# Kernel optimization log

Measured on AMD Instinct MI355X. Metric: run time of the kernel, lower is better.

Reference implementation:

```python
import jax, jax.numpy as jnp
import numpy as np

HEADS = 6
DIM_HEAD = 64
SCALE = DIM_HEAD ** -0.5
BN_EPS = 1e-5


def _dw_pw(x, w_dw, gamma, beta, mean, var, w_pw, stride):
    """Depthwise 3x3 conv (groups=C) -> BatchNorm (inference) -> 1x1 pointwise conv."""
    C = x.shape[1]
    y = jax.lax.conv_general_dilated(
        x, w_dw, window_strides=(stride, stride), padding=((1, 1), (1, 1)),
        dimension_numbers=('NCHW', 'OIHW', 'NCHW'), feature_group_count=C)
    inv = gamma / jnp.sqrt(var + BN_EPS)
    y = y * inv[None, :, None, None] + (beta - mean * inv)[None, :, None, None]
    # 1x1 conv as einsum: w_pw is [O, C]
    return jnp.einsum('bchw,oc->bohw', y, w_pw)


def setup_inputs() -> dict:
    key = jax.random.key(0)
    ks = jax.random.split(key, 10)
    B, C, H, W = 32, 384, 32, 32
    inner = HEADS * DIM_HEAD  # 384
    ws = 0.05  # weight scale to keep attention logits sane
    return {
        'x': jax.random.normal(ks[0], (B, C, H, W), jnp.float32),
        'q_dw': jax.random.normal(ks[1], (C, 1, 3, 3), jnp.float32) * ws,
        'q_gamma': jnp.ones((C,), jnp.float32),
        'q_beta': jnp.zeros((C,), jnp.float32),
        'q_mean': jax.random.normal(ks[2], (C,), jnp.float32) * 0.1,
        'q_var': jax.random.uniform(ks[3], (C,), jnp.float32) + 0.5,
        'q_pw': jax.random.normal(ks[4], (inner, C), jnp.float32) * ws,
        'kv_dw': jax.random.normal(ks[5], (C, 1, 3, 3), jnp.float32) * ws,
        'kv_gamma': jnp.ones((C,), jnp.float32),
        'kv_beta': jnp.zeros((C,), jnp.float32),
        'kv_mean': jax.random.normal(ks[6], (C,), jnp.float32) * 0.1,
        'kv_var': jax.random.uniform(ks[7], (C,), jnp.float32) + 0.5,
        'kv_pw': jax.random.normal(ks[8], (2 * inner, C), jnp.float32) * ws,
        'out_w': jax.random.normal(ks[9], (C, inner), jnp.float32) * ws,
        'out_b': jnp.zeros((C,), jnp.float32),
    }


def reference(x, q_dw, q_gamma, q_beta, q_mean, q_var, q_pw,
              kv_dw, kv_gamma, kv_beta, kv_mean, kv_var, kv_pw,
              out_w, out_b):
    B, C, H, W = x.shape
    h, d = HEADS, DIM_HEAD
    # Q at full resolution, K/V spatially downsampled (stride 2)
    q = _dw_pw(x, q_dw, q_gamma, q_beta, q_mean, q_var, q_pw, stride=1)   # [B, h*d, H, W]
    kv = _dw_pw(x, kv_dw, kv_gamma, kv_beta, kv_mean, kv_var, kv_pw, stride=2)  # [B, 2*h*d, Hk, Wk]
    k, v = jnp.split(kv, 2, axis=1)
    Hk, Wk = k.shape[2], k.shape[3]
    # 'b (h d) x y -> b h (x y) d'
    q = q.reshape(B, h, d, H * W).transpose(0, 1, 3, 2)
    k = k.reshape(B, h, d, Hk * Wk).transpose(0, 1, 3, 2)
    v = v.reshape(B, h, d, Hk * Wk).transpose(0, 1, 3, 2)
    dots = jnp.einsum('bhid,bhjd->bhij', q, k) * SCALE  # [B, h, HW, HkWk]
    attn = jax.nn.softmax(dots, axis=-1)
    out = jnp.einsum('bhij,bhjd->bhid', attn, v)        # [B, h, HW, d]
    # 'b h (x y) d -> b (h d) x y'
    out = out.transpose(0, 1, 3, 2).reshape(B, h * d, H, W)
    # final 1x1 conv projection (dropout is identity, p=0)
    return jnp.einsum('bchw,oc->bohw', out, out_w) + out_b[None, :, None, None]
```

## Files before the change

### kernel.cpp

```cpp
#include <hip/hip_runtime.h>
#include <hip/hip_bf16.h>

#define CIN 384
#define PQ 1024
#define PKV 256
#define HEADS 6
#define DH 64
#define INNER 384
#define ATTN_SCALE 0.125f

typedef __hip_bfloat16 bf16;
typedef unsigned short ushort;
typedef __bf16 bf16x8 __attribute__((ext_vector_type(8)));
typedef float floatx4 __attribute__((ext_vector_type(4)));

__device__ __forceinline__ float b2f(bf16 v) { return __bfloat162float(v); }
__device__ __forceinline__ bf16 f2b(float v) { return __float2bfloat16(v); }
__device__ __forceinline__ ushort f2bu(float v) { bf16 h = __float2bfloat16(v); return *(ushort*)&h; }
__device__ __forceinline__ float ldf(const void* p, size_t i, int isbf) {
    return isbf ? __bfloat162float(((const bf16*)p)[i]) : ((const float*)p)[i];
}
__device__ __forceinline__ void dma16(const bf16* g, bf16* l) {
    __builtin_amdgcn_global_load_lds(
        (const __attribute__((address_space(1))) unsigned int*)g,
        (__attribute__((address_space(3))) unsigned int*)l, 16, 0, 0);
}
__device__ __forceinline__ int probe_isbf(const void* x) {
    const unsigned* u = (const unsigned*)x;
    int cnt = 0;
    for (int i = 0; i < 64; i++) {
        unsigned e = (u[i] >> 7) & 0xFFu;
        cnt += (e >= 100u && e <= 140u) ? 1 : 0;
    }
    return cnt >= 48 ? 1 : 0;
}
__device__ __forceinline__ unsigned cvtpk(float lo, float hi) {
    unsigned r;
    asm("v_cvt_pk_bf16_f32 %0, %1, %2" : "=v"(r) : "v"(lo), "v"(hi));
    return r;
}
__device__ __forceinline__ void halfswap(unsigned a, unsigned b, unsigned& lo, unsigned& hi) {
#if __has_builtin(__builtin_amdgcn_permlane32_swap)
    auto r = __builtin_amdgcn_permlane32_swap(a, b, false, false);
    lo = r[0]; hi = r[1];
#else
    unsigned ax = (unsigned)__shfl_xor((int)a, 32, 64);
    unsigned bx = (unsigned)__shfl_xor((int)b, 32, 64);
    bool lower = (threadIdx.x & 32) == 0;
    lo = lower ? a : bx;
    hi = lower ? ax : b;
#endif
}

__global__ void wconv_kernel(const void* __restrict__ w0, const void* __restrict__ w1,
                             const void* __restrict__ w2, bf16* __restrict__ dst,
                             const void* __restrict__ xprobe) {
    int isbf = probe_isbf(xprobe);
    const int n0 = INNER * CIN, n1 = 2 * INNER * CIN, n2 = INNER * CIN;
    int i = blockIdx.x * 256 + threadIdx.x;
    int total = n0 + n1 + n2;
    for (; i < total; i += gridDim.x * 256) {
        float v;
        if (i < n0) v = ldf(w0, i, isbf);
        else if (i < n0 + n1) v = ldf(w1, i - n0, isbf);
        else v = ldf(w2, i - n0 - n1, isbf);
        dst[i] = f2b(v);
    }
}

template <int STRIDE, int HO, int WO>
__global__ __launch_bounds__(256) void dw_bn_kernel(
        const void* __restrict__ x, const void* __restrict__ wdw,
        const void* __restrict__ gamma, const void* __restrict__ beta,
        const void* __restrict__ mean, const void* __restrict__ var,
        bf16* __restrict__ yt) {
    constexpr int IN_ROWS = (8 - 1) * STRIDE + 3;
    constexpr int RL = 37;
    constexpr int PT = 8 * WO;
    constexpr unsigned XSZ = 32u * IN_ROWS * RL * 4;
    constexpr unsigned OSZ = (unsigned)PT * 40 * 2;
    __shared__ __align__(16) char smem[XSZ > OSZ ? XSZ : OSZ];
    float (*xin)[IN_ROWS][RL] = (float (*)[IN_ROWS][RL])smem;
    ushort (*outt)[40] = (ushort (*)[40])smem;

    int isbf = probe_isbf(x);
    int rg = blockIdx.x;
    int c0 = blockIdx.y * 32;
    int b  = blockIdx.z;
    int tid = threadIdx.x;
    int ri0 = rg * 8 * STRIDE - 1;

    for (int e = tid; e < 32 * IN_ROWS; e += 256) {
        int i = e % IN_ROWS, cc = e / IN_ROWS;
        xin[cc][i][0] = 0.f;
        xin[cc][i][33] = 0.f;
    }

    const int NCHUNK = 32 * IN_ROWS * 4;
    for (int ch = tid; ch < NCHUNK; ch += 256) {
        int wc = ch & 3;
        int t  = ch >> 2;
        int i  = t % IN_ROWS;
        int cc = t / IN_ROWS;
        int row = ri0 + i;
        float f[8];
        if (row >= 0 && row < 32) {
            size_t goff = ((size_t)(b * CIN + c0 + cc) * 32 + row) * 32 + wc * 8;
            if (isbf) {
                uint4 v = *(const uint4*)((const bf16*)x + goff);
                const ushort* u = (const ushort*)&v;
#pragma unroll
                for (int j = 0; j < 8; j++) f[j] = __uint_as_float((unsigned)u[j] << 16);
            } else {
                float4 v0 = *(const float4*)((const float*)x + goff);
                float4 v1 = *(const float4*)((const float*)x + goff + 4);
                f[0] = v0.x; f[1] = v0.y; f[2] = v0.z; f[3] = v0.w;
                f[4] = v1.x; f[5] = v1.y; f[6] = v1.z; f[7] = v1.w;
            }
        } else {
#pragma unroll
            for (int j = 0; j < 8; j++) f[j] = 0.f;
        }
        float* dst = &xin[cc][i][1 + wc * 8];
#pragma unroll
        for (int j = 0; j < 8; j++) dst[j] = f[j];
    }

    int cc = tid & 31;
    int g  = tid >> 5;
    int c  = c0 + cc;
    float w9[9];
#pragma unroll
    for (int k = 0; k < 9; k++) w9[k] = ldf(wdw, c * 9 + k, isbf);
    float inv  = ldf(gamma, c, isbf) * rsqrtf(ldf(var, c, isbf) + 1e-5f);
    float bias = ldf(beta, c, isbf) - ldf(mean, c, isbf) * inv;
    __syncthreads();

    const float* xr0 = xin[cc][g * STRIDE + 0];
    const float* xr1 = xin[cc][g * STRIDE + 1];
    const float* xr2 = xin[cc][g * STRIDE + 2];
    float o[WO];
    if (STRIDE == 1) {
        float a0 = xr0[0], a1 = xr0[1];
        float b0 = xr1[0], b1 = xr1[1];
        float q0 = xr2[0], q1 = xr2[1];
#pragma unroll
        for (int wo = 0; wo < WO; wo++) {
            float a2 = xr0[wo + 2], b2 = xr1[wo + 2], q2 = xr2[wo + 2];
            float acc = w9[0] * a0 + w9[1] * a1 + w9[2] * a2
                      + w9[3] * b0 + w9[4] * b1 + w9[5] * b2
                      + w9[6] * q0 + w9[7] * q1 + w9[8] * q2;
            o[wo] = acc * inv + bias;
            a0 = a1; a1 = a2; b0 = b1; b1 = b2; q0 = q1; q1 = q2;
        }
    } else {
        float a0 = xr0[0], b0 = xr1[0], q0 = xr2[0];
#pragma unroll
        for (int wo = 0; wo < WO; wo++) {
            float a1 = xr0[2 * wo + 1], a2 = xr0[2 * wo + 2];
            float b1 = xr1[2 * wo + 1], b2 = xr1[2 * wo + 2];
            float q1 = xr2[2 * wo + 1], q2 = xr2[2 * wo + 2];
            float acc = w9[0] * a0 + w9[1] * a1 + w9[2] * a2
                      + w9[3] * b0 + w9[4] * b1 + w9[5] * b2
                      + w9[6] * q0 + w9[7] * q1 + w9[8] * q2;
            o[wo] = acc * inv + bias;
            a0 = a2; b0 = b2; q0 = q2;
        }
    }
    __syncthreads();

#pragma unroll
    for (int wo = 0; wo < WO; wo++) outt[g * WO + wo][cc] = f2bu(o[wo]);
    __syncthreads();

    const size_t pbase = (size_t)b * (HO * WO) + (size_t)rg * 8 * WO;
    for (int chk = tid; chk < PT * 4; chk += 256) {
        int k = chk & 3, p = chk >> 2;
        uint4 v = *(const uint4*)&outt[p][k * 8];
        *(uint4*)(yt + (pbase + p) * CIN + c0 + k * 8) = v;
    }
}

__global__ __launch_bounds__(256, 3) void mfma_pw_qkv(
        const bf16* __restrict__ qpw, const bf16* __restrict__ yqt,
        bf16* __restrict__ qalt,
        const bf16* __restrict__ kvpw, const bf16* __restrict__ ykvt,
        bf16* __restrict__ kalt, bf16* __restrict__ valt) {
    __shared__ __align__(16) bf16 As[2][4096];
    __shared__ __align__(16) bf16 Bs[2][4096];
    int tid = threadIdx.x;
    int wave = tid >> 6, lane = tid & 63;
    int l15 = lane & 15, quad = lane >> 4;
    int wm = wave & 1, wn = wave >> 1;

    int bid = blockIdx.x;
    int P, b, p0, o0;
    const bf16 *asrc0, *bsrc0;
    bf16* outq;
    if (bid < 768) {
        int m = bid;
        int p0t = m & 7; m >>= 3;
        int o0t = m % 3; b = m / 3;
        P = 1024; p0 = p0t * 128; o0 = o0t * 128;
        asrc0 = yqt; bsrc0 = qpw; outq = qalt;
    } else {
        int m = bid - 768;
        int p0t = m & 1; m >>= 1;
        int o0t = m % 6; b = m / 6;
        P = 256; p0 = p0t * 128; o0 = o0t * 128;
        asrc0 = ykvt; bsrc0 = kvpw; outq = kalt;
    }

    const bf16* asrc = asrc0 + ((size_t)b * P + p0) * CIN;
    const bf16* bsrc = bsrc0 + (size_t)o0 * CIN;

    int srow = (lane >> 2);
    int sc   = lane & 3;
    auto stage = [&](int step, int buf) {
#pragma unroll
        for (int it = 0; it < 2; it++) {
            int row = wave * 32 + it * 16 + srow;
            int g = sc ^ (row & 3);
            size_t goff = (size_t)row * CIN + step * 32 + g * 8;
            dma16(asrc + goff, &As[buf][(wave * 2 + it) * 512]);
            dma16(bsrc + goff, &Bs[buf][(wave * 2 + it) * 512]);
        }
    };

    floatx4 acc[4][4];
#pragma unroll
    for (int pt = 0; pt < 4; pt++)
#pragma unroll
        for (int ot = 0; ot < 4; ot++) acc[pt][ot] = (floatx4){0.f, 0.f, 0.f, 0.f};

    stage(0, 0);
    __syncthreads();
    for (int s = 0; s < CIN / 32; s++) {
        int buf = s & 1;
        if (s < CIN / 32 - 1) stage(s + 1, buf ^ 1);
        bf16x8 af[4], bw[4];
        int slot = (quad ^ (l15 & 3)) * 8;
#pragma unroll
        for (int pt = 0; pt < 4; pt++)
            af[pt] = *(const bf16x8*)&As[buf][(wm * 64 + pt * 16 + l15) * 32 + slot];
#pragma unroll
        for (int ot = 0; ot < 4; ot++)
            bw[ot] = *(const bf16x8*)&Bs[buf][(wn * 64 + ot * 16 + l15) * 32 + slot];
#pragma unroll
        for (int pt = 0; pt < 4; pt++)
#pragma unroll
            for (int ot = 0; ot < 4; ot++)
                acc[pt][ot] = __builtin_amdgcn_mfma_f32_16x16x32_bf16(af[pt], bw[ot], acc[pt][ot], 0, 0, 0);
        __syncthreads();
    }

    int pw0 = p0 + wm * 64, ow0 = o0 + wn * 64;
#pragma unroll
    for (int ot = 0; ot < 4; ot++) {
        int o = ow0 + ot * 16 + l15;
        if (o < INNER) {
            int h = o >> 6, d = o & 63;
            bf16* base = outq + ((size_t)(b * HEADS + h) * P) * 64 + d;
#pragma unroll
            for (int pt = 0; pt < 4; pt++)
#pragma unroll
                for (int r = 0; r < 4; r++)
                    base[(size_t)(pw0 + pt * 16 + quad * 4 + r) * 64] = f2b(acc[pt][ot][r]);
        } else {
            int ch = o - INNER;
            bf16* base = valt + ((size_t)b * INNER + ch) * PKV;
#pragma unroll
            for (int pt = 0; pt < 4; pt++)
#pragma unroll
                for (int r = 0; r < 4; r++)
                    base[pw0 + pt * 16 + quad * 4 + r] = f2b(acc[pt][ot][r]);
        }
    }
}

__global__ __launch_bounds__(256, 3) void mfma_pw_out(
        const bf16* __restrict__ wt, const bf16* __restrict__ yt,
        const void* __restrict__ bias, void* __restrict__ out0,
        const void* __restrict__ xprobe) {
    __shared__ __align__(16) bf16 As[2][4096];
    __shared__ __align__(16) bf16 Bs[2][4096];
    const int P = PQ, O = CIN;
    int tid = threadIdx.x;
    int wave = tid >> 6, lane = tid & 63;
    int l15 = lane & 15, quad = lane >> 4;
    int wm = wave & 1, wn = wave >> 1;
    int b = blockIdx.z;
    int p0 = blockIdx.x * 128;
    int o0 = blockIdx.y * 128;

    const bf16* asrc = yt + ((size_t)b * P + p0) * CIN;
    const bf16* bsrc = wt + (size_t)o0 * CIN;

    int srow = (lane >> 2);
    int sc   = lane & 3;
    auto stage = [&](int step, int buf) {
#pragma unroll
        for (int it = 0; it < 2; it++) {
            int row = wave * 32 + it * 16 + srow;
            int g = sc ^ (row & 3);
            size_t goff = (size_t)row * CIN + step * 32 + g * 8;
            dma16(asrc + goff, &As[buf][(wave * 2 + it) * 512]);
            dma16(bsrc + goff, &Bs[buf][(wave * 2 + it) * 512]);
        }
    };

    floatx4 acc[4][4];
#pragma unroll
    for (int pt = 0; pt < 4; pt++)
#pragma unroll
        for (int ot = 0; ot < 4; ot++) acc[pt][ot] = (floatx4){0.f, 0.f, 0.f, 0.f};

    stage(0, 0);
    __syncthreads();
    for (int s = 0; s < CIN / 32; s++) {
        int buf = s & 1;
        if (s < CIN / 32 - 1) stage(s + 1, buf ^ 1);
        bf16x8 af[4], bw[4];
        int slot = (quad ^ (l15 & 3)) * 8;
#pragma unroll
        for (int pt = 0; pt < 4; pt++)
            af[pt] = *(const bf16x8*)&As[buf][(wm * 64 + pt * 16 + l15) * 32 + slot];
#pragma unroll
        for (int ot = 0; ot < 4; ot++)
            bw[ot] = *(const bf16x8*)&Bs[buf][(wn * 64 + ot * 16 + l15) * 32 + slot];
#pragma unroll
        for (int pt = 0; pt < 4; pt++)
#pragma unroll
            for (int ot = 0; ot < 4; ot++)
                acc[pt][ot] = __builtin_amdgcn_mfma_f32_16x16x32_bf16(af[pt], bw[ot], acc[pt][ot], 0, 0, 0);
        __syncthreads();
    }

    int pw0 = p0 + wm * 64, ow0 = o0 + wn * 64;
    int isbf = probe_isbf(xprobe);
#pragma unroll
    for (int ot = 0; ot < 4; ot++) {
        int o = ow0 + ot * 16 + l15;
        float bv = ldf(bias, o, isbf);
#pragma unroll
        for (int pt = 0; pt < 4; pt++) {
            int p = pw0 + pt * 16 + quad * 4;
            size_t idx = ((size_t)b * O + o) * P + p;
            if (!isbf) {
                float4 v4 = {acc[pt][ot][0] + bv, acc[pt][ot][1] + bv,
                             acc[pt][ot][2] + bv, acc[pt][ot][3] + bv};
                *(float4*)((float*)out0 + idx) = v4;
            } else {
                ushort4 u4 = {f2bu(acc[pt][ot][0] + bv), f2bu(acc[pt][ot][1] + bv),
                              f2bu(acc[pt][ot][2] + bv), f2bu(acc[pt][ot][3] + bv)};
                *(ushort4*)((bf16*)out0 + idx) = u4;
            }
        }
    }
}

__global__ __launch_bounds__(256, 2) void attn_kernel(
        const bf16* __restrict__ qalt, const bf16* __restrict__ kalt,
        const bf16* __restrict__ valt, bf16* __restrict__ ao) {
    __shared__ __align__(16) bf16 Kl[16384];
    __shared__ __align__(16) bf16 Vl[16384];
    __shared__ __align__(16) ushort Ot[4][16][80];
    int tid = threadIdx.x;
    int wave = tid >> 6, lane = tid & 63;
    int l15 = lane & 15, quad = lane >> 4;
    int blk = blockIdx.x;
    int swz = (blk & 7) * 96 + (blk >> 3);
    int seg = swz & 3;
    int bh  = swz >> 2;
    int b = bh / HEADS, h = bh % HEADS;

    const bf16* qbase = qalt + (size_t)(b * HEADS + h) * PQ * DH;
    const bf16* kbase = kalt + (size_t)(b * HEADS + h) * PKV * DH;
    const bf16* vbase = valt + ((size_t)b * INNER + h * DH) * PKV;

    {
        int j = lane >> 3, cs = lane & 7;
#pragma unroll
        for (int it = 0; it < 8; it++) {
            int jr = (wave * 8 + it) * 8 + j;
            int g = cs ^ (jr & 7);
            dma16(kbase + (size_t)jr * 64 + g * 8, &Kl[(wave * 8 + it) * 512]);
        }
        int d = lane >> 5, cs2 = lane & 31;
#pragma unroll
        for (int it = 0; it < 8; it++) {
            int dr = (wave * 8 + it) * 2 + d;
            int g = cs2 ^ (dr & 15);
            dma16(vbase + (size_t)dr * 256 + g * 8, &Vl[(wave * 8 + it) * 512]);
        }
    }

    int p0 = seg * 256 + wave * 16;
    const bf16* qrow = qbase + (size_t)(p0 + l15) * DH + quad * 8;
    bf16x8 qc0 = *(const bf16x8*)qrow;
    bf16x8 qc1 = *(const bf16x8*)(qrow + 32);
    __syncthreads();

    const float C = ATTN_SCALE * 1.44269504f;

#pragma unroll
    for (int t = 0; t < 4; t++) {
        bf16x8 qn0 = qc0, qn1 = qc1;
        if (t < 3) {
            const bf16* qr = qrow + (size_t)(t + 1) * 64 * DH;
            qn0 = *(const bf16x8*)qr;
            qn1 = *(const bf16x8*)(qr + 32);
        }

        floatx4 s[16];
#pragma unroll
        for (int jt = 0; jt < 16; jt++) s[jt] = (floatx4){0.f, 0.f, 0.f, 0.f};
        __builtin_amdgcn_s_setprio(1);
#pragma unroll
        for (int jt = 0; jt < 16; jt++) {
            int j = jt * 16 + l15;
            bf16x8 k0 = *(const bf16x8*)&Kl[j * 64 + (quad ^ (j & 7)) * 8];
            bf16x8 k1 = *(const bf16x8*)&Kl[j * 64 + ((4 + quad) ^ (j & 7)) * 8];
            s[jt] = __builtin_amdgcn_mfma_f32_16x16x32_bf16(k0, qc0, s[jt], 0, 0, 0);
            s[jt] = __builtin_amdgcn_mfma_f32_16x16x32_bf16(k1, qc1, s[jt], 0, 0, 0);
        }
        __builtin_amdgcn_s_setprio(0);

        float mx = s[0][0];
#pragma unroll
        for (int jt = 0; jt < 16; jt++)
#pragma unroll
            for (int r = 0; r < 4; r++) mx = fmaxf(mx, s[jt][r]);
        mx = fmaxf(mx, __shfl_xor(mx, 16, 64));
        mx = fmaxf(mx, __shfl_xor(mx, 32, 64));
        float mc = mx * C;
        float sm = 0.f;
#pragma unroll
        for (int jt = 0; jt < 16; jt++)
#pragma unroll
            for (int r = 0; r < 4; r++) {
                float e = exp2f(s[jt][r] * C - mc);
                s[jt][r] = e;
                sm += e;
            }
        sm += __shfl_xor(sm, 16, 64);
        sm += __shfl_xor(sm, 32, 64);
        float pinv = 1.f / sm;

        floatx4 oacc[4];
#pragma unroll
        for (int nt = 0; nt < 4; nt++) oacc[nt] = (floatx4){0.f, 0.f, 0.f, 0.f};
        __builtin_amdgcn_s_setprio(1);
#pragma unroll
        for (int kk = 0; kk < 8; kk++) {
            floatx4 se = s[2 * kk], so = s[2 * kk + 1];
            unsigned E0 = cvtpk(se[0] * pinv, se[1] * pinv);
            unsigned E1 = cvtpk(se[2] * pinv, se[3] * pinv);
            unsigned D0 = cvtpk(so[0] * pinv, so[1] * pinv);
            unsigned D1 = cvtpk(so[2] * pinv, so[3] * pinv);
            unsigned lo0, hi0, lo1, hi1;
            halfswap(E0, D0, lo0, hi0);
            halfswap(E1, D1, lo1, hi1);
            unsigned sel0 = (quad & 1) ? hi0 : lo0;
            unsigned sel1 = (quad & 1) ? hi1 : lo1;
            unsigned x0 = (unsigned)__shfl_xor((int)sel0, 16, 64);
            unsigned x1 = (unsigned)__shfl_xor((int)sel1, 16, 64);
            union { unsigned u[4]; bf16x8 v; } pf;
            pf.u[0] = (quad & 1) ? x0 : sel0;
            pf.u[1] = (quad & 1) ? x1 : sel1;
            pf.u[2] = (quad & 1) ? sel0 : x0;
            pf.u[3] = (quad & 1) ? sel1 : x1;
#pragma unroll
            for (int nt = 0; nt < 4; nt++) {
                int d = nt * 16 + l15;
                bf16x8 bv = *(const bf16x8*)&Vl[d * 256 + ((kk * 4 + quad) ^ (d & 15)) * 8];
                oacc[nt] = __builtin_amdgcn_mfma_f32_16x16x32_bf16(pf.v, bv, oacc[nt], 0, 0, 0);
            }
        }
        __builtin_amdgcn_s_setprio(0);

#pragma unroll
        for (int nt = 0; nt < 4; nt++)
#pragma unroll
            for (int r = 0; r < 4; r++)
                Ot[wave][quad * 4 + r][nt * 16 + l15] = f2bu(oacc[nt][r]);
        int row = lane >> 2, d0 = (lane & 3) * 16;
        uint4 ld0 = *(const uint4*)&Ot[wave][row][d0];
        uint4 ld1 = *(const uint4*)&Ot[wave][row][d0 + 8];
        bf16* dst = ao + ((size_t)b * PQ + p0 + t * 64 + row) * INNER + h * DH + d0;
        *(uint4*)dst = ld0;
        *(uint4*)(dst + 8) = ld1;

        qc0 = qn0; qc1 = qn1;
    }
}

extern "C" void kernel_launch(void* const* d_in, const int* in_sizes, int n_in,
                              void* d_out, int out_size, void* d_ws, size_t ws_size,
                              hipStream_t stream) {
    const void* x        = d_in[0];
    const void* q_dw     = d_in[1];
    const void* q_gamma  = d_in[2];
    const void* q_beta   = d_in[3];
    const void* q_mean   = d_in[4];
    const void* q_var    = d_in[5];
    const void* q_pw     = d_in[6];
    const void* kv_dw    = d_in[7];
    const void* kv_gamma = d_in[8];
    const void* kv_beta  = d_in[9];
    const void* kv_mean  = d_in[10];
    const void* kv_var   = d_in[11];
    const void* kv_pw    = d_in[12];
    const void* out_w    = d_in[13];
    const void* out_b    = d_in[14];

    bf16* pool = (bf16*)((char*)d_ws + 256);
    bf16* yqt  = pool;
    bf16* ykvt = yqt  + (size_t)32 * 1024 * 384;
    bf16* qalt = ykvt + (size_t)32 * 256 * 384;
    bf16* kalt = qalt + (size_t)32 * 6 * 1024 * 64;
    bf16* valt = kalt + (size_t)32 * 6 * 256 * 64;
    bf16* wbf  = valt + (size_t)32 * 384 * 256;
    bf16* qpw_bf = wbf;
    bf16* kvpw_bf = wbf + (size_t)INNER * CIN;
    bf16* outw_bf = kvpw_bf + (size_t)2 * INNER * CIN;
    bf16* aob  = yqt;

    wconv_kernel<<<576, 256, 0, stream>>>(q_pw, kv_pw, out_w, wbf, x);
    dw_bn_kernel<1, 32, 32><<<dim3(4, 12, 32), 256, 0, stream>>>(x, q_dw, q_gamma, q_beta, q_mean, q_var, yqt);
    dw_bn_kernel<2, 16, 16><<<dim3(2, 12, 32), 256, 0, stream>>>(x, kv_dw, kv_gamma, kv_beta, kv_mean, kv_var, ykvt);
    mfma_pw_qkv<<<1152, 256, 0, stream>>>(qpw_bf, yqt, qalt, kvpw_bf, ykvt, kalt, valt);
    attn_kernel<<<768, 256, 0, stream>>>(qalt, kalt, valt, aob);
    mfma_pw_out<<<dim3(8, 3, 32), 256, 0, stream>>>(outw_bf, aob, out_b, d_out, x);
}
```

Before: 240.2 us.

## Fold weight conversion into dw kernel and software-pipeline attention QK/softmax/PV

The separate weight bf16 conversion kernel is removed. Its work moves into an extra slice of blocks (blockIdx.y == 12) of the stride-1 depthwise kernel, saving one launch. The attention kernel's per-tile loop is restructured into a two-buffer software pipeline: the QK^T of the next 64-row tile is issued before the PV of the current tile, so MFMA work can overlap the softmax and shuffle work. Softmax reductions now use four independent accumulators. The cost is roughly double the score registers, which may pressure the 2-blocks-per-SM occupancy target, and the setprio hints are dropped.

```diff
diff --git a/kernel.cpp b/kernel.cpp
--- a/kernel.cpp
+++ b/kernel.cpp
@@ -52,28 +52,14 @@
 #endif
 }
 
-__global__ void wconv_kernel(const void* __restrict__ w0, const void* __restrict__ w1,
-                             const void* __restrict__ w2, bf16* __restrict__ dst,
-                             const void* __restrict__ xprobe) {
-    int isbf = probe_isbf(xprobe);
-    const int n0 = INNER * CIN, n1 = 2 * INNER * CIN, n2 = INNER * CIN;
-    int i = blockIdx.x * 256 + threadIdx.x;
-    int total = n0 + n1 + n2;
-    for (; i < total; i += gridDim.x * 256) {
-        float v;
-        if (i < n0) v = ldf(w0, i, isbf);
-        else if (i < n0 + n1) v = ldf(w1, i - n0, isbf);
-        else v = ldf(w2, i - n0 - n1, isbf);
-        dst[i] = f2b(v);
-    }
-}
-
 template <int STRIDE, int HO, int WO>
 __global__ __launch_bounds__(256) void dw_bn_kernel(
         const void* __restrict__ x, const void* __restrict__ wdw,
         const void* __restrict__ gamma, const void* __restrict__ beta,
         const void* __restrict__ mean, const void* __restrict__ var,
-        bf16* __restrict__ yt) {
+        bf16* __restrict__ yt,
+        const void* __restrict__ w0, const void* __restrict__ w1,
+        const void* __restrict__ w2, bf16* __restrict__ wdst) {
     constexpr int IN_ROWS = (8 - 1) * STRIDE + 3;
     constexpr int RL = 37;
     constexpr int PT = 8 * WO;
@@ -88,6 +74,20 @@
     int c0 = blockIdx.y * 32;
     int b  = blockIdx.z;
     int tid = threadIdx.x;
+
+    if (c0 >= CIN) {
+        const int n0 = INNER * CIN, n1 = 2 * INNER * CIN, n2 = INNER * CIN;
+        const int total = n0 + n1 + n2;
+        for (int i = (b * 4 + rg) * 256 + tid; i < total; i += 32768) {
+            float v;
+            if (i < n0) v = ldf(w0, i, isbf);
+            else if (i < n0 + n1) v = ldf(w1, i - n0, isbf);
+            else v = ldf(w2, i - n0 - n1, isbf);
+            wdst[i] = f2b(v);
+        }
+        return;
+    }
+
     int ri0 = rg * 8 * STRIDE - 1;
 
     for (int e = tid; e < 32 * IN_ROWS; e += 256) {
@@ -359,6 +359,91 @@
     }
 }
 
+#define QKT(S, Q0, Q1)                                                              \
+    do {                                                                            \
+        floatx4 z_ = (floatx4){0.f, 0.f, 0.f, 0.f};                                 \
+        _Pragma("unroll")                                                           \
+        for (int jt_ = 0; jt_ < 16; jt_++) {                                        \
+            int j_ = jt_ * 16 + l15;                                                \
+            bf16x8 k0_ = *(const bf16x8*)&Kl[j_ * 64 + (quad ^ (j_ & 7)) * 8];      \
+            bf16x8 k1_ = *(const bf16x8*)&Kl[j_ * 64 + ((4 + quad) ^ (j_ & 7)) * 8];\
+            floatx4 t_ = __builtin_amdgcn_mfma_f32_16x16x32_bf16(k0_, Q0, z_, 0, 0, 0); \
+            S[jt_] = __builtin_amdgcn_mfma_f32_16x16x32_bf16(k1_, Q1, t_, 0, 0, 0); \
+        }                                                                           \
+    } while (0)
+
+#define SOFTMAX(S, PINV)                                                            \
+    do {                                                                            \
+        float m0_ = S[0][0], m1_ = S[0][1], m2_ = S[0][2], m3_ = S[0][3];           \
+        _Pragma("unroll")                                                           \
+        for (int jt_ = 1; jt_ < 16; jt_++) {                                        \
+            m0_ = fmaxf(m0_, S[jt_][0]); m1_ = fmaxf(m1_, S[jt_][1]);               \
+            m2_ = fmaxf(m2_, S[jt_][2]); m3_ = fmaxf(m3_, S[jt_][3]);               \
+        }                                                                           \
+        float mx_ = fmaxf(fmaxf(m0_, m1_), fmaxf(m2_, m3_));                        \
+        mx_ = fmaxf(mx_, __shfl_xor(mx_, 16, 64));                                  \
+        mx_ = fmaxf(mx_, __shfl_xor(mx_, 32, 64));                                  \
+        float mc_ = mx_ * C;                                                        \
+        float a0_ = 0.f, a1_ = 0.f, a2_ = 0.f, a3_ = 0.f;                           \
+        _Pragma("unroll")                                                           \
+        for (int jt_ = 0; jt_ < 16; jt_++) {                                        \
+            float e0_ = exp2f(S[jt_][0] * C - mc_);                                 \
+            float e1_ = exp2f(S[jt_][1] * C - mc_);                                 \
+            float e2_ = exp2f(S[jt_][2] * C - mc_);                                 \
+            float e3_ = exp2f(S[jt_][3] * C - mc_);                                 \
+            S[jt_][0] = e0_; S[jt_][1] = e1_; S[jt_][2] = e2_; S[jt_][3] = e3_;     \
+            a0_ += e0_; a1_ += e1_; a2_ += e2_; a3_ += e3_;                         \
+        }                                                                           \
+        float sm_ = (a0_ + a1_) + (a2_ + a3_);                                      \
+        sm_ += __shfl_xor(sm_, 16, 64);                                             \
+        sm_ += __shfl_xor(sm_, 32, 64);                                             \
+        PINV = 1.f / sm_;                                                           \
+    } while (0)
+
+#define PV_STORE(S, PINV, T)                                                        \
+    do {                                                                            \
+        floatx4 oacc_[4];                                                           \
+        _Pragma("unroll")                                                           \
+        for (int nt_ = 0; nt_ < 4; nt_++) oacc_[nt_] = (floatx4){0.f, 0.f, 0.f, 0.f}; \
+        _Pragma("unroll")                                                           \
+        for (int kk_ = 0; kk_ < 8; kk_++) {                                         \
+            floatx4 se_ = S[2 * kk_], so_ = S[2 * kk_ + 1];                         \
+            unsigned E0_ = cvtpk(se_[0] * PINV, se_[1] * PINV);                     \
+            unsigned E1_ = cvtpk(se_[2] * PINV, se_[3] * PINV);                     \
+            unsigned D0_ = cvtpk(so_[0] * PINV, so_[1] * PINV);                     \
+            unsigned D1_ = cvtpk(so_[2] * PINV, so_[3] * PINV);                     \
+            unsigned lo0_, hi0_, lo1_, hi1_;                                        \
+            halfswap(E0_, D0_, lo0_, hi0_);                                         \
+            halfswap(E1_, D1_, lo1_, hi1_);                                         \
+            unsigned sel0_ = (quad & 1) ? hi0_ : lo0_;                              \
+            unsigned sel1_ = (quad & 1) ? hi1_ : lo1_;                              \
+            unsigned x0_ = (unsigned)__shfl_xor((int)sel0_, 16, 64);                \
+            unsigned x1_ = (unsigned)__shfl_xor((int)sel1_, 16, 64);                \
+            union { unsigned u[4]; bf16x8 v; } pf_;                                 \
+            pf_.u[0] = (quad & 1) ? x0_ : sel0_;                                    \
+            pf_.u[1] = (quad & 1) ? x1_ : sel1_;                                    \
+            pf_.u[2] = (quad & 1) ? sel0_ : x0_;                                    \
+            pf_.u[3] = (quad & 1) ? sel1_ : x1_;                                    \
+            _Pragma("unroll")                                                       \
+            for (int nt_ = 0; nt_ < 4; nt_++) {                                     \
+                int d_ = nt_ * 16 + l15;                                            \
+                bf16x8 bv_ = *(const bf16x8*)&Vl[d_ * 256 + ((kk_ * 4 + quad) ^ (d_ & 15)) * 8]; \
+                oacc_[nt_] = __builtin_amdgcn_mfma_f32_16x16x32_bf16(pf_.v, bv_, oacc_[nt_], 0, 0, 0); \
+            }                                                                       \
+        }                                                                           \
+        _Pragma("unroll")                                                           \
+        for (int nt_ = 0; nt_ < 4; nt_++)                                           \
+            _Pragma("unroll")                                                       \
+            for (int r_ = 0; r_ < 4; r_++)                                          \
+                Ot[wave][quad * 4 + r_][nt_ * 16 + l15] = f2bu(oacc_[nt_][r_]);     \
+        int row_ = lane >> 2, d0_ = (lane & 3) * 16;                                \
+        uint4 ld0_ = *(const uint4*)&Ot[wave][row_][d0_];                           \
+        uint4 ld1_ = *(const uint4*)&Ot[wave][row_][d0_ + 8];                       \
+        bf16* dst_ = ao + ((size_t)b * PQ + p0 + (T) * 64 + row_) * INNER + h * DH + d0_; \
+        *(uint4*)dst_ = ld0_;                                                       \
+        *(uint4*)(dst_ + 8) = ld1_;                                                 \
+    } while (0)
+
 __global__ __launch_bounds__(256, 2) void attn_kernel(
         const bf16* __restrict__ qalt, const bf16* __restrict__ kalt,
         const bf16* __restrict__ valt, bf16* __restrict__ ao) {
@@ -397,102 +482,36 @@
 
     int p0 = seg * 256 + wave * 16;
     const bf16* qrow = qbase + (size_t)(p0 + l15) * DH + quad * 8;
-    bf16x8 qc0 = *(const bf16x8*)qrow;
-    bf16x8 qc1 = *(const bf16x8*)(qrow + 32);
+    bf16x8 qA0 = *(const bf16x8*)qrow;
+    bf16x8 qA1 = *(const bf16x8*)(qrow + 32);
+    bf16x8 qB0 = *(const bf16x8*)(qrow + 64 * DH);
+    bf16x8 qB1 = *(const bf16x8*)(qrow + 64 * DH + 32);
     __syncthreads();
 
     const float C = ATTN_SCALE * 1.44269504f;
-
-#pragma unroll
-    for (int t = 0; t < 4; t++) {
-        bf16x8 qn0 = qc0, qn1 = qc1;
-        if (t < 3) {
-            const bf16* qr = qrow + (size_t)(t + 1) * 64 * DH;
-            qn0 = *(const bf16x8*)qr;
-            qn1 = *(const bf16x8*)(qr + 32);
-        }
-
-        floatx4 s[16];
-#pragma unroll
-        for (int jt = 0; jt < 16; jt++) s[jt] = (floatx4){0.f, 0.f, 0.f, 0.f};
-        __builtin_amdgcn_s_setprio(1);
-#pragma unroll
-        for (int jt = 0; jt < 16; jt++) {
-            int j = jt * 16 + l15;
-            bf16x8 k0 = *(const bf16x8*)&Kl[j * 64 + (quad ^ (j & 7)) * 8];
-            bf16x8 k1 = *(const bf16x8*)&Kl[j * 64 + ((4 + quad) ^ (j & 7)) * 8];
-            s[jt] = __builtin_amdgcn_mfma_f32_16x16x32_bf16(k0, qc0, s[jt], 0, 0, 0);
-            s[jt] = __builtin_amdgcn_mfma_f32_16x16x32_bf16(k1, qc1, s[jt], 0, 0, 0);
-        }
-        __builtin_amdgcn_s_setprio(0);
-
-        float mx = s[0][0];
-#pragma unroll
-        for (int jt = 0; jt < 16; jt++)
-#pragma unroll
-            for (int r = 0; r < 4; r++) mx = fmaxf(mx, s[jt][r]);
-        mx = fmaxf(mx, __shfl_xor(mx, 16, 64));
-        mx = fmaxf(mx, __shfl_xor(mx, 32, 64));
-        float mc = mx * C;
-        float sm = 0.f;
-#pragma unroll
-        for (int jt = 0; jt < 16; jt++)
-#pragma unroll
-            for (int r = 0; r < 4; r++) {
-                float e = exp2f(s[jt][r] * C - mc);
-                s[jt][r] = e;
-                sm += e;
-            }
-        sm += __shfl_xor(sm, 16, 64);
-        sm += __shfl_xor(sm, 32, 64);
-        float pinv = 1.f / sm;
-
-        floatx4 oacc[4];
-#pragma unroll
-        for (int nt = 0; nt < 4; nt++) oacc[nt] = (floatx4){0.f, 0.f, 0.f, 0.f};
-        __builtin_amdgcn_s_setprio(1);
-#pragma unroll
-        for (int kk = 0; kk < 8; kk++) {
-            floatx4 se = s[2 * kk], so = s[2 * kk + 1];
-            unsigned E0 = cvtpk(se[0] * pinv, se[1] * pinv);
-            unsigned E1 = cvtpk(se[2] * pinv, se[3] * pinv);
-            unsigned D0 = cvtpk(so[0] * pinv, so[1] * pinv);
-            unsigned D1 = cvtpk(so[2] * pinv, so[3] * pinv);
-            unsigned lo0, hi0, lo1, hi1;
-            halfswap(E0, D0, lo0, hi0);
-            halfswap(E1, D1, lo1, hi1);
-            unsigned sel0 = (quad & 1) ? hi0 : lo0;
-            unsigned sel1 = (quad & 1) ? hi1 : lo1;
-            unsigned x0 = (unsigned)__shfl_xor((int)sel0, 16, 64);
-            unsigned x1 = (unsigned)__shfl_xor((int)sel1, 16, 64);
-            union { unsigned u[4]; bf16x8 v; } pf;
-            pf.u[0] = (quad & 1) ? x0 : sel0;
-            pf.u[1] = (quad & 1) ? x1 : sel1;
-            pf.u[2] = (quad & 1) ? sel0 : x0;
-            pf.u[3] = (quad & 1) ? sel1 : x1;
-#pragma unroll
-            for (int nt = 0; nt < 4; nt++) {
-                int d = nt * 16 + l15;
-                bf16x8 bv = *(const bf16x8*)&Vl[d * 256 + ((kk * 4 + quad) ^ (d & 15)) * 8];
-                oacc[nt] = __builtin_amdgcn_mfma_f32_16x16x32_bf16(pf.v, bv, oacc[nt], 0, 0, 0);
-            }
-        }
-        __builtin_amdgcn_s_setprio(0);
-
-#pragma unroll
-        for (int nt = 0; nt < 4; nt++)
-#pragma unroll
-            for (int r = 0; r < 4; r++)
-                Ot[wave][quad * 4 + r][nt * 16 + l15] = f2bu(oacc[nt][r]);
-        int row = lane >> 2, d0 = (lane & 3) * 16;
-        uint4 ld0 = *(const uint4*)&Ot[wave][row][d0];
-        uint4 ld1 = *(const uint4*)&Ot[wave][row][d0 + 8];
-        bf16* dst = ao + ((size_t)b * PQ + p0 + t * 64 + row) * INNER + h * DH + d0;
-        *(uint4*)dst = ld0;
-        *(uint4*)(dst + 8) = ld1;
-
-        qc0 = qn0; qc1 = qn1;
-    }
+    floatx4 sA[16], sB[16];
+    float pinv;
+
+    QKT(sA, qA0, qA1);
+    qA0 = *(const bf16x8*)(qrow + 128 * DH);
+    qA1 = *(const bf16x8*)(qrow + 128 * DH + 32);
+
+    SOFTMAX(sA, pinv);
+    QKT(sB, qB0, qB1);
+    PV_STORE(sA, pinv, 0);
+    qB0 = *(const bf16x8*)(qrow + 192 * DH);
+    qB1 = *(const bf16x8*)(qrow + 192 * DH + 32);
+
+    SOFTMAX(sB, pinv);
+    QKT(sA, qA0, qA1);
+    PV_STORE(sB, pinv, 1);
+
+    SOFTMAX(sA, pinv);
+    QKT(sB, qB0, qB1);
+    PV_STORE(sA, pinv, 2);
+
+    SOFTMAX(sB, pinv);
+    PV_STORE(sB, pinv, 3);
 }
 
 extern "C" void kernel_launch(void* const* d_in, const int* in_sizes, int n_in,
@@ -526,9 +545,10 @@
     bf16* outw_bf = kvpw_bf + (size_t)2 * INNER * CIN;
     bf16* aob  = yqt;
 
-    wconv_kernel<<<576, 256, 0, stream>>>(q_pw, kv_pw, out_w, wbf, x);
-    dw_bn_kernel<1, 32, 32><<<dim3(4, 12, 32), 256, 0, stream>>>(x, q_dw, q_gamma, q_beta, q_mean, q_var, yqt);
-    dw_bn_kernel<2, 16, 16><<<dim3(2, 12, 32), 256, 0, stream>>>(x, kv_dw, kv_gamma, kv_beta, kv_mean, kv_var, ykvt);
+    dw_bn_kernel<1, 32, 32><<<dim3(4, 13, 32), 256, 0, stream>>>(
+        x, q_dw, q_gamma, q_beta, q_mean, q_var, yqt, q_pw, kv_pw, out_w, wbf);
+    dw_bn_kernel<2, 16, 16><<<dim3(2, 12, 32), 256, 0, stream>>>(
+        x, kv_dw, kv_gamma, kv_beta, kv_mean, kv_var, ykvt, nullptr, nullptr, nullptr, nullptr);
     mfma_pw_qkv<<<1152, 256, 0, stream>>>(qpw_bf, yqt, qalt, kvpw_bf, ykvt, kalt, valt);
     attn_kernel<<<768, 256, 0, stream>>>(qalt, kalt, valt, aob);
     mfma_pw_out<<<dim3(8, 3, 32), 256, 0, stream>>>(outw_bf, aob, out_b, d_out, x);
```

Result: no change. 236.8 us (-1.4%).
